# Optimization experiments

Hardware: AMD Instinct MI355X
Metric: run time of the kernel (lower is better)

Reference implementation:

```python
import jax, jax.numpy as jnp
import numpy as np

NUM_CLASSES = 80
ROI_SIZE = 7
SAMPLING = 2          # RoIAlign sampling_ratio
STRIDES = (4, 8, 16, 32)
FINEST_SCALE = 56.0
SCORE_THR = 0.05
IOU_THR = 0.5
MAX_PER_IMG = 100
MEANS = jnp.zeros((4,), jnp.float32)
STDS = jnp.array([0.1, 0.1, 0.2, 0.2], jnp.float32)
MAX_RATIO = abs(float(np.log(16.0 / 1000.0)))


def setup_inputs() -> dict:
    key = jax.random.key(0)
    ks = jax.random.split(key, 20)
    C, H0, W0 = 256, 200, 336
    inp = {}
    for i in range(4):
        inp[f"feat{i}"] = jax.random.normal(ks[i], (1, C, H0 >> i, W0 >> i), jnp.float32)
    N = 1000
    IMG_W, IMG_H = 1344.0, 800.0
    cx = jax.random.uniform(ks[4], (N,), minval=0.0, maxval=IMG_W)
    cy = jax.random.uniform(ks[5], (N,), minval=0.0, maxval=IMG_H)
    w = jax.random.uniform(ks[6], (N,), minval=16.0, maxval=512.0)
    h = jax.random.uniform(ks[7], (N,), minval=16.0, maxval=512.0)
    x1 = jnp.clip(cx - w / 2, 0.0, IMG_W - 1)
    y1 = jnp.clip(cy - h / 2, 0.0, IMG_H - 1)
    x2 = jnp.clip(cx + w / 2, x1 + 1.0, IMG_W)
    y2 = jnp.clip(cy + h / 2, y1 + 1.0, IMG_H)
    inp["proposals"] = jnp.stack([x1, y1, x2, y2], axis=-1)
    D = C * ROI_SIZE * ROI_SIZE  # 12544
    FC = 1024
    inp["fc1_w"] = 0.01 * jax.random.normal(ks[8], (FC, D), jnp.float32)
    inp["fc1_b"] = jnp.zeros((FC,), jnp.float32)
    inp["fc2_w"] = 0.01 * jax.random.normal(ks[9], (FC, FC), jnp.float32)
    inp["fc2_b"] = jnp.zeros((FC,), jnp.float32)
    inp["cls_w"] = 0.01 * jax.random.normal(ks[10], (NUM_CLASSES + 1, FC), jnp.float32)
    inp["cls_b"] = jnp.zeros((NUM_CLASSES + 1,), jnp.float32)
    inp["reg_w"] = 0.01 * jax.random.normal(ks[11], (NUM_CLASSES * 4, FC), jnp.float32)
    inp["reg_b"] = jnp.zeros((NUM_CLASSES * 4,), jnp.float32)
    return inp


def _roi_align(feat, rois, scale):
    # feat [C,H,W]; rois [N,4]; aligned RoIAlign, 7x7 out, sampling_ratio=2
    C, H, W = feat.shape
    P = ROI_SIZE * SAMPLING  # 14 uniform sample points per axis

    def one(roi):
        x1, y1, x2, y2 = roi[0], roi[1], roi[2], roi[3]
        sx = x1 * scale - 0.5
        sy = y1 * scale - 0.5
        rw = (x2 - x1) * scale
        rh = (y2 - y1) * scale
        pts = (jnp.arange(P, dtype=feat.dtype) + 0.5) / P
        xs = sx + pts * rw
        ys = sy + pts * rh
        y0 = jnp.floor(ys)
        x0 = jnp.floor(xs)
        ly = ys - y0
        lx = xs - x0
        y0i = jnp.clip(y0.astype(jnp.int32), 0, H - 1)
        y1i = jnp.clip(y0i + 1, 0, H - 1)
        x0i = jnp.clip(x0.astype(jnp.int32), 0, W - 1)
        x1i = jnp.clip(x0i + 1, 0, W - 1)
        g = lambda yi, xi: feat[:, yi[:, None], xi[None, :]]  # [C,P,P]
        ly_ = ly[None, :, None]
        lx_ = lx[None, None, :]
        val = (1 - ly_) * ((1 - lx_) * g(y0i, x0i) + lx_ * g(y0i, x1i)) \
            + ly_ * ((1 - lx_) * g(y1i, x0i) + lx_ * g(y1i, x1i))
        vy = ((ys >= -1.0) & (ys <= H))[None, :, None]
        vx = ((xs >= -1.0) & (xs <= W))[None, None, :]
        val = jnp.where(vy & vx, val, 0.0)
        # average-pool the 2x2 samples per bin -> [C,7,7]
        return val.reshape(C, ROI_SIZE, SAMPLING, ROI_SIZE, SAMPLING).mean(axis=(2, 4))

    return jax.vmap(one)(rois)  # [N,C,7,7]


def _delta2bbox(proposals, deltas):
    d = deltas.reshape(-1, NUM_CLASSES, 4) * STDS + MEANS
    dx, dy = d[..., 0], d[..., 1]
    dw = jnp.clip(d[..., 2], -MAX_RATIO, MAX_RATIO)
    dh = jnp.clip(d[..., 3], -MAX_RATIO, MAX_RATIO)
    px = ((proposals[:, 0] + proposals[:, 2]) * 0.5)[:, None]
    py = ((proposals[:, 1] + proposals[:, 3]) * 0.5)[:, None]
    pw = (proposals[:, 2] - proposals[:, 0])[:, None]
    ph = (proposals[:, 3] - proposals[:, 1])[:, None]
    gw = pw * jnp.exp(dw)
    gh = ph * jnp.exp(dh)
    gx = px + pw * dx
    gy = py + ph * dy
    return jnp.stack([gx - gw * 0.5, gy - gh * 0.5, gx + gw * 0.5, gy + gh * 0.5], axis=-1)


def _pairwise_iou(b):
    x1, y1, x2, y2 = b[:, 0], b[:, 1], b[:, 2], b[:, 3]
    area = jnp.maximum(x2 - x1, 0.0) * jnp.maximum(y2 - y1, 0.0)
    iw = jnp.maximum(jnp.minimum(x2[:, None], x2[None, :]) - jnp.maximum(x1[:, None], x1[None, :]), 0.0)
    ih = jnp.maximum(jnp.minimum(y2[:, None], y2[None, :]) - jnp.maximum(y1[:, None], y1[None, :]), 0.0)
    inter = iw * ih
    return inter / jnp.maximum(area[:, None] + area[None, :] - inter, 1e-8)


def _nms_one_class(boxes, scores):
    # greedy NMS, static shapes; returns score-sorted boxes/scores + keep mask
    N = scores.shape[0]
    order = jnp.argsort(-scores)
    b = boxes[order]
    s = scores[order]
    iou = _pairwise_iou(b)
    idx = jnp.arange(N)

    def body(i, keep):
        sup = (iou[i] > IOU_THR) & keep[i] & (idx > i)
        return keep & jnp.logical_not(sup)

    keep = jax.lax.fori_loop(0, N, body, s > SCORE_THR)
    return b, s, keep


def _batched_nms(bboxes, scores):
    # bboxes [N,81,4], scores [N,81]; class 80 is background (skipped)
    cls_boxes = jnp.transpose(bboxes[:, :NUM_CLASSES, :], (1, 0, 2))  # [80,N,4]
    cls_scores = scores[:, :NUM_CLASSES].T                            # [80,N]
    b, s, keep = jax.vmap(_nms_one_class)(cls_boxes, cls_scores)
    N = s.shape[1]
    s_flat = jnp.where(keep, s, -1.0).reshape(-1)
    topv, topi = jax.lax.top_k(s_flat, MAX_PER_IMG)
    det_boxes = b.reshape(-1, 4)[topi]
    det_classes = (topi // N).astype(jnp.int32)
    valid = topv > 0.0
    num_det = valid.sum().astype(jnp.int32)
    det_scores = jnp.where(valid, topv, 0.0)
    det_boxes = jnp.where(valid[:, None], det_boxes, 0.0)
    det_classes = jnp.where(valid, det_classes, -1)
    return num_det, det_boxes[None], det_scores[None], det_classes[None]


def _forward(feat0, feat1, feat2, feat3, proposals,
             fc1_w, fc1_b, fc2_w, fc2_b, cls_w, cls_b, reg_w, reg_b):
    feats = [feat0[0], feat1[0], feat2[0], feat3[0]]
    wp = proposals[:, 2] - proposals[:, 0]
    hp = proposals[:, 3] - proposals[:, 1]
    scale = jnp.sqrt(jnp.maximum(wp * hp, 1e-6))
    lvl = jnp.clip(jnp.floor(jnp.log2(scale / FINEST_SCALE + 1e-6)), 0, 3).astype(jnp.int32)
    N = proposals.shape[0]
    C = feats[0].shape[0]
    roi_feats = jnp.zeros((N, C, ROI_SIZE, ROI_SIZE), proposals.dtype)
    for l, stride in enumerate(STRIDES):
        f = _roi_align(feats[l], proposals, 1.0 / stride)
        roi_feats = jnp.where((lvl == l)[:, None, None, None], f, roi_feats)
    h = roi_feats.reshape(N, -1)
    h = jax.nn.relu(h @ fc1_w.T + fc1_b)
    h = jax.nn.relu(h @ fc2_w.T + fc2_b)
    cls_score = h @ cls_w.T + cls_b          # [N,81]
    bbox_pred = h @ reg_w.T + reg_b          # [N,320]
    scores = jax.nn.softmax(cls_score, axis=1)
    boxes = _delta2bbox(proposals, bbox_pred)                          # [N,80,4]
    boxes = jnp.concatenate([boxes, jnp.zeros((N, 1, 4), boxes.dtype)], axis=1)
    return _batched_nms(boxes, scores)


def reference(feat0, feat1, feat2, feat3, proposals,
              fc1_w, fc1_b, fc2_w, fc2_b, cls_w, cls_b, reg_w, reg_b):
    return _forward(feat0, feat1, feat2, feat3, proposals,
                    fc1_w, fc1_b, fc2_w, fc2_b, cls_w, cls_b, reg_w, reg_b)
```

## Files before the change

### kernel.cpp

```cpp
#include <hip/hip_runtime.h>
#include <math.h>

#define NCLS   80
#define NPROP  1000
#define FCDIM  1024
#define DFLAT  12544
#define MPAD   1024
#define MAXR   4.1351665567423560f
#define LDSP   40
#define NMSW   16
#define NCAT   404

#define CSPLIT 8
#define CG     (256 / CSPLIT)

typedef unsigned short ushort_t;
typedef unsigned long long ull_t;
using short8  = __attribute__((ext_vector_type(8))) short;
using float4v = __attribute__((ext_vector_type(4))) float;

__device__ inline ushort_t f2bf(float f) {
    unsigned int u = __float_as_uint(f);
    unsigned int r = (u + 0x7fffu + ((u >> 16) & 1u)) >> 16;
    return (ushort_t)r;
}

__device__ __forceinline__ unsigned cvtpk_bf16(float lo, float hi) {
    unsigned r;
    asm("v_cvt_pk_bf16_f32 %0, %1, %2" : "=v"(r) : "v"(lo), "v"(hi));
    return r;
}

__global__ __launch_bounds__(256) void roi_align_k(
    const float* __restrict__ f0, const float* __restrict__ f1,
    const float* __restrict__ f2, const float* __restrict__ f3,
    const float* __restrict__ props, ushort_t* __restrict__ Abf)
{
    int r  = blockIdx.x;
    int cz = blockIdx.y;
    int t  = threadIdx.x;

    if (r >= NPROP) {
        for (int i = t; i < CG * 49; i += 256)
            Abf[(size_t)r * DFLAT + cz * (CG * 49) + i] = 0;
        return;
    }

    const float4 p = *(const float4*)&props[(size_t)r * 4];
    float wp = p.z - p.x, hp = p.w - p.y;
    float scale = sqrtf(fmaxf(wp * hp, 1e-6f));
    int lvl = (int)floorf(log2f(scale / 56.0f + 1e-6f));
    lvl = min(max(lvl, 0), 3);

    const float* f; int H, W; float sc;
    switch (lvl) {
        case 0:  f = f0; H = 200; W = 336; sc = 0.25f;    break;
        case 1:  f = f1; H = 100; W = 168; sc = 0.125f;   break;
        case 2:  f = f2; H = 50;  W = 84;  sc = 0.0625f;  break;
        default: f = f3; H = 25;  W = 42;  sc = 0.03125f; break;
    }

    if (t >= 196) return;

    int b   = t >> 2;
    int sub = t & 3;
    int by = b / 7, bx = b - by * 7;
    int sy = by * 2 + (sub >> 1);
    int sx = bx * 2 + (sub & 1);

    float startx = p.x * sc - 0.5f, rangex = (p.z - p.x) * sc;
    float starty = p.y * sc - 0.5f, rangey = (p.w - p.y) * sc;
    float posx = startx + (((float)sx + 0.5f) / 14.0f) * rangex;
    float posy = starty + (((float)sy + 0.5f) / 14.0f) * rangey;

    float flx = floorf(posx), fly = floorf(posy);
    float lx = posx - flx, ly = posy - fly;
    int x0 = min(max((int)flx, 0), W - 1);
    int y0 = min(max((int)fly, 0), H - 1);
    int y1 = min(y0 + 1, H - 1);
    bool valid = (posx >= -1.0f) && (posx <= (float)W) &&
                 (posy >= -1.0f) && (posy <= (float)H);
    float vm = valid ? 0.25f : 0.0f;

    float w00 = (1.f - ly) * (1.f - lx) * vm;
    float w01 = (1.f - ly) * lx * vm;
    float w10 = ly * (1.f - lx) * vm;
    float w11 = ly * lx * vm;

    int  xb = min(x0, W - 2);
    bool xr = (x0 == W - 1);
    float wtA = xr ? 0.f : w00, wtB = xr ? (w00 + w01) : w01;
    float wbA = xr ? 0.f : w10, wbB = xr ? (w10 + w11) : w11;
    int ot = y0 * W + xb;
    int ob = y1 * W + xb;

    const int HW = H * W;
    ushort_t* orow = Abf + (size_t)r * DFLAT + cz * (CG * 49);
    const float* pl = f + (size_t)(cz * CG) * HW;

    #pragma unroll 8
    for (int c = 0; c < CG; c++) {
        float2 tv = *(const float2*)(pl + ot);
        float2 bv = *(const float2*)(pl + ob);
        float v = tv.x * wtA + tv.y * wtB + bv.x * wbA + bv.y * wbB;
        v += __shfl_xor(v, 1);
        v += __shfl_xor(v, 2);
        if (sub == 0)
            orow[c * 49 + b] = f2bf(v);
        pl += HW;
    }
}

__global__ __launch_bounds__(256) void gemm_sk_k(
    const ushort_t* __restrict__ A, const float* __restrict__ Wf,
    float* __restrict__ P, int N, int K, int KC)
{
    __shared__ ushort_t As[2][128 * LDSP];
    __shared__ ushort_t Bs[2][128 * LDSP];

    int tid = threadIdx.x;
    int w = tid >> 6, l = tid & 63;
    int wm = (w >> 1) * 64, wn = (w & 1) * 64;

    int bid = (int)blockIdx.x + (int)gridDim.x * ((int)blockIdx.y + (int)gridDim.y * (int)blockIdx.z);
    int bx = bid & 7;
    int slot = bid >> 3;
    int by = slot % (int)gridDim.y;
    int bz = slot / (int)gridDim.y;

    int m0 = by * 128, n0 = bx * 128;
    int kc0 = bz * KC;

    int lrow = tid >> 2;
    int lko  = (tid & 3) * 8;

    const ushort_t* Ag = A  + (size_t)(m0 + lrow) * K + kc0 + lko;
    const float*    Wg = Wf + (size_t)(n0 + lrow) * K + kc0 + lko;
    size_t rowK64 = (size_t)64 * K;

    float4v acc[4][4];
    #pragma unroll
    for (int i = 0; i < 4; i++)
        #pragma unroll
        for (int j = 0; j < 4; j++)
            acc[i][j] = (float4v){0.f, 0.f, 0.f, 0.f};

    int rl = l & 15, q = l >> 4;

    {
        uint4  a0  = *(const uint4*)(Ag);
        uint4  a1  = *(const uint4*)(Ag + rowK64);
        float4 w0a = *(const float4*)(Wg);
        float4 w0b = *(const float4*)(Wg + 4);
        float4 w1a = *(const float4*)(Wg + rowK64);
        float4 w1b = *(const float4*)(Wg + rowK64 + 4);
        uint4 wv0, wv1;
        wv0.x = cvtpk_bf16(w0a.x, w0a.y); wv0.y = cvtpk_bf16(w0a.z, w0a.w);
        wv0.z = cvtpk_bf16(w0b.x, w0b.y); wv0.w = cvtpk_bf16(w0b.z, w0b.w);
        wv1.x = cvtpk_bf16(w1a.x, w1a.y); wv1.y = cvtpk_bf16(w1a.z, w1a.w);
        wv1.z = cvtpk_bf16(w1b.x, w1b.y); wv1.w = cvtpk_bf16(w1b.z, w1b.w);
        *(uint4*)&As[0][lrow * LDSP + lko]        = a0;
        *(uint4*)&As[0][(lrow + 64) * LDSP + lko] = a1;
        *(uint4*)&Bs[0][lrow * LDSP + lko]        = wv0;
        *(uint4*)&Bs[0][(lrow + 64) * LDSP + lko] = wv1;
    }
    __syncthreads();

    int cur = 0;
    for (int k0 = 0; k0 < KC; k0 += 32) {
        bool more = (k0 + 32) < KC;

        uint4 na0, na1;
        float4 nw0a, nw0b, nw1a, nw1b;
        if (more) {
            na0  = *(const uint4*)(Ag + k0 + 32);
            na1  = *(const uint4*)(Ag + rowK64 + k0 + 32);
            nw0a = *(const float4*)(Wg + k0 + 32);
            nw0b = *(const float4*)(Wg + k0 + 36);
            nw1a = *(const float4*)(Wg + rowK64 + k0 + 32);
            nw1b = *(const float4*)(Wg + rowK64 + k0 + 36);
        }

        const ushort_t* Ac = As[cur];
        const ushort_t* Bc = Bs[cur];
        short8 af[4], bfr[4];
        #pragma unroll
        for (int i = 0; i < 4; i++)
            af[i] = *(const short8*)&Ac[(wm + i * 16 + rl) * LDSP + q * 8];
        #pragma unroll
        for (int j = 0; j < 4; j++)
            bfr[j] = *(const short8*)&Bc[(wn + j * 16 + rl) * LDSP + q * 8];

        #pragma unroll
        for (int i = 0; i < 4; i++)
            #pragma unroll
            for (int j = 0; j < 4; j++)
                acc[i][j] = __builtin_amdgcn_mfma_f32_16x16x32_bf16(
                    af[i], bfr[j], acc[i][j], 0, 0, 0);

        if (more) {
            uint4 wv0, wv1;
            wv0.x = cvtpk_bf16(nw0a.x, nw0a.y); wv0.y = cvtpk_bf16(nw0a.z, nw0a.w);
            wv0.z = cvtpk_bf16(nw0b.x, nw0b.y); wv0.w = cvtpk_bf16(nw0b.z, nw0b.w);
            wv1.x = cvtpk_bf16(nw1a.x, nw1a.y); wv1.y = cvtpk_bf16(nw1a.z, nw1a.w);
            wv1.z = cvtpk_bf16(nw1b.x, nw1b.y); wv1.w = cvtpk_bf16(nw1b.z, nw1b.w);
            ushort_t* An = As[cur ^ 1];
            ushort_t* Bn = Bs[cur ^ 1];
            *(uint4*)&An[lrow * LDSP + lko]        = na0;
            *(uint4*)&An[(lrow + 64) * LDSP + lko] = na1;
            *(uint4*)&Bn[lrow * LDSP + lko]        = wv0;
            *(uint4*)&Bn[(lrow + 64) * LDSP + lko] = wv1;
        }

        __syncthreads();
        cur ^= 1;
    }

    float* Pz = P + (size_t)bz * ((size_t)MPAD * N);
    #pragma unroll
    for (int i = 0; i < 4; i++) {
        #pragma unroll
        for (int j = 0; j < 4; j++) {
            int col = n0 + wn + j * 16 + rl;
            #pragma unroll
            for (int rr = 0; rr < 4; rr++) {
                int row = m0 + wm + i * 16 + q * 4 + rr;
                Pz[(size_t)row * N + col] = acc[i][j][rr];
            }
        }
    }
}

__global__ __launch_bounds__(256) void reduce_sk_k(
    const float* __restrict__ P, const float* __restrict__ bias,
    void* __restrict__ Cout, int N, int SK, int relu, int out_bf16)
{
    size_t idx = ((size_t)blockIdx.x * 256 + threadIdx.x) * 4;
    float4 s = *(const float4*)&P[idx];
    for (int z = 1; z < SK; z++) {
        float4 pv = *(const float4*)&P[(size_t)z * ((size_t)MPAD * N) + idx];
        s.x += pv.x; s.y += pv.y; s.z += pv.z; s.w += pv.w;
    }
    int n = (int)(idx % N);
    float4 b = *(const float4*)&bias[n];
    s.x += b.x; s.y += b.y; s.z += b.z; s.w += b.w;
    if (relu) {
        s.x = fmaxf(s.x, 0.f); s.y = fmaxf(s.y, 0.f);
        s.z = fmaxf(s.z, 0.f); s.w = fmaxf(s.w, 0.f);
    }
    if (out_bf16) {
        ushort4 o;
        o.x = f2bf(s.x); o.y = f2bf(s.y); o.z = f2bf(s.z); o.w = f2bf(s.w);
        *(ushort4*)&((ushort_t*)Cout)[idx] = o;
    } else {
        *(float4*)&((float*)Cout)[idx] = s;
    }
}

__global__ __launch_bounds__(256) void concat_w_k(
    const float* __restrict__ reg_w, const float* __restrict__ cls_w,
    const float* __restrict__ reg_b, const float* __restrict__ cls_b,
    float* __restrict__ Wcat, float* __restrict__ bcat)
{
    int row = blockIdx.x;
    int t = threadIdx.x;
    float4 v = make_float4(0.f, 0.f, 0.f, 0.f);
    float bv = 0.f;
    if (row < 320) {
        v = *(const float4*)&reg_w[(size_t)row * FCDIM + t * 4];
        bv = reg_b[row];
    } else if (row < NCAT - 3) {
        v = *(const float4*)&cls_w[(size_t)(row - 320) * FCDIM + t * 4];
        bv = cls_b[row - 320];
    }
    *(float4*)&Wcat[(size_t)row * FCDIM + t * 4] = v;
    if (t == 0) bcat[row] = bv;
}

__global__ __launch_bounds__(256) void gemm_tn_k(
    const float* __restrict__ A, const float* __restrict__ W,
    const float* __restrict__ bias, float* __restrict__ C,
    int M, int N, int K, int relu)
{
    __shared__ float As[16][64];
    __shared__ float Bs[16][64];

    int tid = threadIdx.x;
    int tx = tid & 15;
    int ty = tid >> 4;
    int m0 = blockIdx.y * 64, n0 = blockIdx.x * 64;

    int lr = tid >> 2;
    int lk = (tid & 3) << 2;

    const float* Arow = A + (size_t)(m0 + lr) * K + lk;
    const float* Wrow = W + (size_t)(n0 + lr) * K + lk;
    bool mOK = (m0 + lr) < M;
    bool nOK = (n0 + lr) < N;

    float acc[4][4] = {};

    for (int k0 = 0; k0 < K; k0 += 16) {
        float4 av = mOK ? *(const float4*)(Arow + k0) : make_float4(0.f, 0.f, 0.f, 0.f);
        float4 wv = nOK ? *(const float4*)(Wrow + k0) : make_float4(0.f, 0.f, 0.f, 0.f);
        As[lk + 0][lr] = av.x; As[lk + 1][lr] = av.y;
        As[lk + 2][lr] = av.z; As[lk + 3][lr] = av.w;
        Bs[lk + 0][lr] = wv.x; Bs[lk + 1][lr] = wv.y;
        Bs[lk + 2][lr] = wv.z; Bs[lk + 3][lr] = wv.w;
        __syncthreads();

        #pragma unroll
        for (int kk = 0; kk < 16; kk++) {
            float4 a = *(const float4*)&As[kk][ty << 2];
            float4 b = *(const float4*)&Bs[kk][tx << 2];
            acc[0][0] += a.x * b.x; acc[0][1] += a.x * b.y;
            acc[0][2] += a.x * b.z; acc[0][3] += a.x * b.w;
            acc[1][0] += a.y * b.x; acc[1][1] += a.y * b.y;
            acc[1][2] += a.y * b.z; acc[1][3] += a.y * b.w;
            acc[2][0] += a.z * b.x; acc[2][1] += a.z * b.y;
            acc[2][2] += a.z * b.z; acc[2][3] += a.z * b.w;
            acc[3][0] += a.w * b.x; acc[3][1] += a.w * b.y;
            acc[3][2] += a.w * b.z; acc[3][3] += a.w * b.w;
        }
        __syncthreads();
    }

    #pragma unroll
    for (int i = 0; i < 4; i++) {
        int m = m0 + (ty << 2) + i;
        if (m >= M) continue;
        #pragma unroll
        for (int j = 0; j < 4; j++) {
            int n = n0 + (tx << 2) + j;
            if (n < N) {
                float v = acc[i][j] + bias[n];
                if (relu) v = fmaxf(v, 0.f);
                C[(size_t)m * N + n] = v;
            }
        }
    }
}

__global__ __launch_bounds__(128) void head_post_k(
    const float* __restrict__ hr_s, const float* __restrict__ props,
    float* __restrict__ probsT, float* __restrict__ boxesT)
{
    int r = blockIdx.x, t = threadIdx.x;
    __shared__ float red[128];

    float x = (t < 81) ? hr_s[(size_t)r * NCAT + 320 + t] : -1e30f;
    red[t] = x; __syncthreads();
    for (int s = 64; s > 0; s >>= 1) {
        if (t < s) red[t] = fmaxf(red[t], red[t + s]);
        __syncthreads();
    }
    float mx = red[0];
    __syncthreads();

    float e = (t < 81) ? expf(x - mx) : 0.f;
    red[t] = e; __syncthreads();
    for (int s = 64; s > 0; s >>= 1) {
        if (t < s) red[t] += red[t + s];
        __syncthreads();
    }
    float inv = 1.f / red[0];

    if (t < NCLS) {
        probsT[(size_t)t * NPROP + r] = e * inv;

        const float4 p = *(const float4*)&props[(size_t)r * 4];
        float4 d = *(const float4*)&hr_s[(size_t)r * NCAT + t * 4];
        float dx = d.x * 0.1f, dy = d.y * 0.1f;
        float dw = fminf(fmaxf(d.z * 0.2f, -MAXR), MAXR);
        float dh = fminf(fmaxf(d.w * 0.2f, -MAXR), MAXR);
        float px = (p.x + p.z) * 0.5f, py = (p.y + p.w) * 0.5f;
        float pw = p.z - p.x, ph = p.w - p.y;
        float gw = pw * expf(dw), gh = ph * expf(dh);
        float gx = px + pw * dx, gy = py + ph * dy;
        float4 bo = make_float4(gx - gw * 0.5f, gy - gh * 0.5f,
                                gx + gw * 0.5f, gy + gh * 0.5f);
        *(float4*)&boxesT[(size_t)(t * NPROP + r) * 4] = bo;
    }
}

__global__ __launch_bounds__(512) void sort_k(
    const float* __restrict__ probsT, const float* __restrict__ boxesT,
    float* __restrict__ sortedS, float* __restrict__ sortedB)
{
    int c = blockIdx.x, t = threadIdx.x;
    __shared__ float sk[1024];
    __shared__ int   si[1024];

    for (int j = t; j < 1024; j += 512) {
        sk[j] = (j < NPROP) ? probsT[(size_t)c * NPROP + j] : -1e30f;
        si[j] = j;
    }
    __syncthreads();

    for (int size = 2; size <= 1024; size <<= 1) {
        for (int stride = size >> 1; stride > 0; stride >>= 1) {
            int i = (t << 1) - (t & (stride - 1));
            int j = i + stride;
            float ka = sk[i], kb = sk[j];
            int ia = si[i], ib = si[j];
            bool aFirst = (ka > kb) || (ka == kb && ia < ib);
            bool desc = ((i & size) == 0);
            if (desc ? !aFirst : aFirst) {
                sk[i] = kb; sk[j] = ka; si[i] = ib; si[j] = ia;
            }
            __syncthreads();
        }
    }

    for (int j = t; j < NPROP; j += 512) {
        sortedS[(size_t)c * NPROP + j] = sk[j];
        const float4 bb = *(const float4*)&boxesT[(size_t)(c * NPROP + si[j]) * 4];
        *(float4*)&sortedB[(size_t)(c * NPROP + j) * 4] = bb;
    }
}

__global__ __launch_bounds__(256) void nms_k(
    const float* __restrict__ sortedS, const float* __restrict__ sortedB,
    ull_t* __restrict__ masks, float* __restrict__ candS, int* __restrict__ candI)
{
    int c = blockIdx.x, t = threadIdx.x;
    __shared__ float x1s[NPROP], y1s[NPROP], x2s[NPROP], y2s[NPROP], ars[NPROP];
    __shared__ unsigned char kp[NPROP];
    __shared__ int segc[256];

    for (int j = t; j < NPROP; j += 256) {
        float4 b = *(const float4*)&sortedB[(size_t)(c * NPROP + j) * 4];
        x1s[j] = b.x; y1s[j] = b.y; x2s[j] = b.z; y2s[j] = b.w;
        ars[j] = fmaxf(b.z - b.x, 0.f) * fmaxf(b.w - b.y, 0.f);
        kp[j] = sortedS[(size_t)c * NPROP + j] > 0.05f ? 1 : 0;
    }
    __syncthreads();

    ull_t* M = masks + (size_t)c * NPROP * NMSW;
    for (int i = t; i < NPROP; i += 256) {
        if (!kp[i]) continue;
        float xi1 = x1s[i], yi1 = y1s[i], xi2 = x2s[i], yi2 = y2s[i], ai = ars[i];
        for (int w = 0; w < NMSW; w++) {
            ull_t m = 0ull;
            int j0 = w << 6;
            #pragma unroll 4
            for (int k = 0; k < 64; k++) {
                int j = j0 + k;
                if (j < NPROP) {
                    float iw = fmaxf(fminf(xi2, x2s[j]) - fmaxf(xi1, x1s[j]), 0.f);
                    float ih = fmaxf(fminf(yi2, y2s[j]) - fmaxf(yi1, y1s[j]), 0.f);
                    float inter = iw * ih;
                    float iou = inter / fmaxf(ai + ars[j] - inter, 1e-8f);
                    if (iou > 0.5f) m |= (1ull << k);
                }
            }
            M[(size_t)i * NMSW + w] = m;
        }
    }
    __syncthreads();

    if (t < 64) {
        ull_t rem = 0ull;
        for (int i = 0; i < NPROP; i++) {
            if (kp[i]) {
                ull_t w = __shfl(rem, i >> 6);
                if ((w >> (i & 63)) & 1ull) {
                    if (t == 0) kp[i] = 0;
                } else {
                    if (t < NMSW) rem |= M[(size_t)i * NMSW + t];
                }
            }
        }
    }
    __syncthreads();

    int j0 = t * 4;
    int cnt = 0;
    #pragma unroll
    for (int k = 0; k < 4; k++) {
        int j = j0 + k;
        if (j < NPROP && kp[j]) cnt++;
    }
    segc[t] = cnt;
    __syncthreads();
    for (int off = 1; off < 256; off <<= 1) {
        int add = (t >= off) ? segc[t - off] : 0;
        __syncthreads();
        segc[t] += add;
        __syncthreads();
    }
    int pos = segc[t] - cnt;
    #pragma unroll
    for (int k = 0; k < 4; k++) {
        int j = j0 + k;
        if (j < NPROP && kp[j]) {
            if (pos < 100) {
                candS[c * 100 + pos] = sortedS[(size_t)c * NPROP + j];
                candI[c * 100 + pos] = c * NPROP + j;
            }
            pos++;
        }
    }
    int total = segc[255];
    for (int p = total + t; p < 100; p += 256) {
        candS[c * 100 + p] = -2e30f;
        candI[c * 100 + p] = 0x7fffffff;
    }
}

__global__ __launch_bounds__(128) void merge_k(
    const float* __restrict__ candS, const int* __restrict__ candI,
    const float* __restrict__ sortedB, float* __restrict__ out)
{
    int t = threadIdx.x;
    __shared__ int   head[NCLS];
    __shared__ float topv[100];
    __shared__ int   topi[100];

    if (t < NCLS) head[t] = 0;
    __syncthreads();

    for (int r = 0; r < 100; r++) {
        if (t < 64) {
            float v = -2e30f; int fi = 0x7fffffff; int cls = 0;
            {
                int h = head[t];
                if (h < 100) { v = candS[t * 100 + h]; fi = candI[t * 100 + h]; cls = t; }
            }
            int c2 = t + 64;
            if (c2 < NCLS) {
                int h = head[c2];
                if (h < 100) {
                    float v2 = candS[c2 * 100 + h]; int fi2 = candI[c2 * 100 + h];
                    if (v2 > v || (v2 == v && fi2 < fi)) { v = v2; fi = fi2; cls = c2; }
                }
            }
            #pragma unroll
            for (int s = 1; s < 64; s <<= 1) {
                float ov = __shfl_xor(v, s);
                int ofi  = __shfl_xor(fi, s);
                int ocl  = __shfl_xor(cls, s);
                if (ov > v || (ov == v && ofi < fi)) { v = ov; fi = ofi; cls = ocl; }
            }
            if (t == 0) { topv[r] = v; topi[r] = fi; head[cls]++; }
        }
        __syncthreads();
    }

    if (t < 100) {
        float v = topv[t]; int fi = topi[t];
        bool valid = v > 0.0f;
        float4 bb = make_float4(0.f, 0.f, 0.f, 0.f);
        if (valid) bb = *(const float4*)&sortedB[(size_t)fi * 4];
        out[1 + t * 4 + 0] = bb.x;
        out[1 + t * 4 + 1] = bb.y;
        out[1 + t * 4 + 2] = bb.z;
        out[1 + t * 4 + 3] = bb.w;
        out[401 + t] = valid ? v : 0.0f;
        out[501 + t] = valid ? (float)(fi / NPROP) : -1.0f;
    }
    if (t == 0) {
        int n = 0;
        for (int r = 0; r < 100; r++) n += (topv[r] > 0.0f) ? 1 : 0;
        out[0] = (float)n;
    }
}

extern "C" void kernel_launch(void* const* d_in, const int* in_sizes, int n_in,
                              void* d_out, int out_size, void* d_ws, size_t ws_size,
                              hipStream_t stream)
{
    const float* f0    = (const float*)d_in[0];
    const float* f1    = (const float*)d_in[1];
    const float* f2    = (const float*)d_in[2];
    const float* f3    = (const float*)d_in[3];
    const float* props = (const float*)d_in[4];
    const float* fc1_w = (const float*)d_in[5];
    const float* fc1_b = (const float*)d_in[6];
    const float* fc2_w = (const float*)d_in[7];
    const float* fc2_b = (const float*)d_in[8];
    const float* cls_w = (const float*)d_in[9];
    const float* cls_b = (const float*)d_in[10];
    const float* reg_w = (const float*)d_in[11];
    const float* reg_b = (const float*)d_in[12];
    float* out = (float*)d_out;

    unsigned char* base = (unsigned char*)d_ws;
    ushort_t* Abf  = (ushort_t*)(base);
    ushort_t* h1   = (ushort_t*)(base + 25690112);
    float*    P1   = (float*)(base + 27787264);
    float*    P2   = (float*)(base + 27787264);
    float*    h2   = (float*)(base + 44564480);
    float*    hr_s    = (float*)(base + 48758784);
    float*    probsT  = (float*)(base + 50401280);
    float*    boxesT  = (float*)(base + 50721280);
    float*    sortedS = (float*)(base + 52001280);
    float*    sortedB = (float*)(base + 52321280);
    float*    candS   = (float*)(base + 53601280);
    int*      candI   = (int*)(base + 53633280);
    float*    Wcat    = (float*)(base + 53665280);
    float*    bcat    = (float*)(base + 55320064);
    ull_t*    masks   = (ull_t*)(base);

    roi_align_k<<<dim3(MPAD, CSPLIT), 256, 0, stream>>>(f0, f1, f2, f3, props, Abf);

    gemm_sk_k<<<dim3(FCDIM / 128, MPAD / 128, 8), 256, 0, stream>>>(
        Abf, fc1_w, P1, FCDIM, DFLAT, DFLAT / 8);
    reduce_sk_k<<<(MPAD * FCDIM / 4) / 256, 256, 0, stream>>>(
        P1, fc1_b, h1, FCDIM, 8, 1, 1);

    concat_w_k<<<NCAT, 256, 0, stream>>>(reg_w, cls_w, reg_b, cls_b, Wcat, bcat);

    gemm_sk_k<<<dim3(FCDIM / 128, MPAD / 128, 4), 256, 0, stream>>>(
        h1, fc2_w, P2, FCDIM, FCDIM, FCDIM / 4);
    reduce_sk_k<<<(MPAD * FCDIM / 4) / 256, 256, 0, stream>>>(
        P2, fc2_b, h2, FCDIM, 4, 1, 0);

    gemm_tn_k<<<dim3((NCAT + 63) / 64, (NPROP + 63) / 64), 256, 0, stream>>>(
        h2, Wcat, bcat, hr_s, NPROP, NCAT, FCDIM, 0);

    head_post_k<<<NPROP, 128, 0, stream>>>(hr_s, props, probsT, boxesT);
    sort_k<<<NCLS, 512, 0, stream>>>(probsT, boxesT, sortedS, sortedB);
    nms_k<<<NCLS, 256, 0, stream>>>(sortedS, sortedB, masks, candS, candI);
    merge_k<<<1, 128, 0, stream>>>(candS, candI, sortedB, out);
}
```

Before: 565.9 us.

## Transpose FPN features to bf16 NHWC before RoIAlign for coalesced channel gathers

Adds a transpose kernel that converts all four feature levels into a channel-last bf16 buffer, done in two 128-channel halves that reuse workspace space. A new RoIAlign kernel precomputes sample offsets and weights in LDS, then has threads read adjacent channels of each bilinear corner, so gathers become coalesced instead of strided across NCHW planes. In exchange, the whole feature pyramid (about 89k pixels by 256 channels) is read and rewritten on every call, and the launch count rises from one to four. Features are rounded to bf16 before interpolation, which adds some precision loss.

```diff
diff --git a/kernel.cpp b/kernel.cpp
--- a/kernel.cpp
+++ b/kernel.cpp
@@ -10,9 +10,8 @@
 #define LDSP   40
 #define NMSW   16
 #define NCAT   404
-
-#define CSPLIT 8
-#define CG     (256 / CSPLIT)
+#define NPIX   89250
+#define HCH    128
 
 typedef unsigned short ushort_t;
 typedef unsigned long long ull_t;
@@ -24,6 +23,9 @@
     unsigned int r = (u + 0x7fffu + ((u >> 16) & 1u)) >> 16;
     return (ushort_t)r;
 }
+__device__ inline float bf2f(ushort_t u) {
+    return __uint_as_float(((unsigned int)u) << 16);
+}
 
 __device__ __forceinline__ unsigned cvtpk_bf16(float lo, float hi) {
     unsigned r;
@@ -31,84 +33,119 @@
     return r;
 }
 
-__global__ __launch_bounds__(256) void roi_align_k(
+__global__ __launch_bounds__(256) void nhwc_k(
     const float* __restrict__ f0, const float* __restrict__ f1,
     const float* __restrict__ f2, const float* __restrict__ f3,
-    const float* __restrict__ props, ushort_t* __restrict__ Abf)
-{
-    int r  = blockIdx.x;
-    int cz = blockIdx.y;
-    int t  = threadIdx.x;
+    int half, ushort_t* __restrict__ Fh)
+{
+    int pt = blockIdx.x;
+    const float* src; int HW, loff, p0;
+    if (pt < 2100)      { src = f0; HW = 67200; loff = 0;     p0 = pt * 32; }
+    else if (pt < 2625) { src = f1; HW = 16800; loff = 67200; p0 = (pt - 2100) * 32; }
+    else if (pt < 2757) { src = f2; HW = 4200;  loff = 84000; p0 = (pt - 2625) * 32; }
+    else                { src = f3; HW = 1050;  loff = 88200; p0 = (pt - 2757) * 32; }
+
+    int tx = threadIdx.x, ty = threadIdx.y;
+    int cbase = half * HCH + blockIdx.y * 32;
+    __shared__ float tile[32][33];
+
+    #pragma unroll
+    for (int i = 0; i < 4; i++) {
+        int cy = ty + i * 8;
+        int p  = p0 + tx;
+        tile[cy][tx] = (p < HW) ? src[(size_t)(cbase + cy) * HW + p] : 0.f;
+    }
+    __syncthreads();
+    #pragma unroll
+    for (int i = 0; i < 4; i++) {
+        int py = ty + i * 8;
+        int p  = p0 + py;
+        if (p < HW)
+            Fh[(size_t)(loff + p) * HCH + blockIdx.y * 32 + tx] = f2bf(tile[tx][py]);
+    }
+}
+
+__global__ __launch_bounds__(256) void roi_nhwc_k(
+    const float* __restrict__ props, const ushort_t* __restrict__ Fh,
+    int half, ushort_t* __restrict__ Abf)
+{
+    int r = blockIdx.x;
+    int t = threadIdx.x;
+    ushort_t* orow = Abf + (size_t)r * DFLAT + half * (HCH * 49);
 
     if (r >= NPROP) {
-        for (int i = t; i < CG * 49; i += 256)
-            Abf[(size_t)r * DFLAT + cz * (CG * 49) + i] = 0;
+        for (int i = t; i < HCH * 49; i += 256) orow[i] = 0;
         return;
     }
 
-    const float4 p = *(const float4*)&props[(size_t)r * 4];
-    float wp = p.z - p.x, hp = p.w - p.y;
-    float scale = sqrtf(fmaxf(wp * hp, 1e-6f));
-    int lvl = (int)floorf(log2f(scale / 56.0f + 1e-6f));
-    lvl = min(max(lvl, 0), 3);
-
-    const float* f; int H, W; float sc;
-    switch (lvl) {
-        case 0:  f = f0; H = 200; W = 336; sc = 0.25f;    break;
-        case 1:  f = f1; H = 100; W = 168; sc = 0.125f;   break;
-        case 2:  f = f2; H = 50;  W = 84;  sc = 0.0625f;  break;
-        default: f = f3; H = 25;  W = 42;  sc = 0.03125f; break;
-    }
-
-    if (t >= 196) return;
-
-    int b   = t >> 2;
-    int sub = t & 3;
-    int by = b / 7, bx = b - by * 7;
-    int sy = by * 2 + (sub >> 1);
-    int sx = bx * 2 + (sub & 1);
-
-    float startx = p.x * sc - 0.5f, rangex = (p.z - p.x) * sc;
-    float starty = p.y * sc - 0.5f, rangey = (p.w - p.y) * sc;
-    float posx = startx + (((float)sx + 0.5f) / 14.0f) * rangex;
-    float posy = starty + (((float)sy + 0.5f) / 14.0f) * rangey;
-
-    float flx = floorf(posx), fly = floorf(posy);
-    float lx = posx - flx, ly = posy - fly;
-    int x0 = min(max((int)flx, 0), W - 1);
-    int y0 = min(max((int)fly, 0), H - 1);
-    int y1 = min(y0 + 1, H - 1);
-    bool valid = (posx >= -1.0f) && (posx <= (float)W) &&
-                 (posy >= -1.0f) && (posy <= (float)H);
-    float vm = valid ? 0.25f : 0.0f;
-
-    float w00 = (1.f - ly) * (1.f - lx) * vm;
-    float w01 = (1.f - ly) * lx * vm;
-    float w10 = ly * (1.f - lx) * vm;
-    float w11 = ly * lx * vm;
-
-    int  xb = min(x0, W - 2);
-    bool xr = (x0 == W - 1);
-    float wtA = xr ? 0.f : w00, wtB = xr ? (w00 + w01) : w01;
-    float wbA = xr ? 0.f : w10, wbB = xr ? (w10 + w11) : w11;
-    int ot = y0 * W + xb;
-    int ob = y1 * W + xb;
-
-    const int HW = H * W;
-    ushort_t* orow = Abf + (size_t)r * DFLAT + cz * (CG * 49);
-    const float* pl = f + (size_t)(cz * CG) * HW;
-
-    #pragma unroll 8
-    for (int c = 0; c < CG; c++) {
-        float2 tv = *(const float2*)(pl + ot);
-        float2 bv = *(const float2*)(pl + ob);
-        float v = tv.x * wtA + tv.y * wtB + bv.x * wbA + bv.y * wbB;
-        v += __shfl_xor(v, 1);
-        v += __shfl_xor(v, 2);
-        if (sub == 0)
-            orow[c * 49 + b] = f2bf(v);
-        pl += HW;
-    }
+    __shared__ int4   offs[196];
+    __shared__ float4 wgts[196];
+    __shared__ ushort_t obuf[HCH * 49];
+
+    if (t < 196) {
+        const float4 p = *(const float4*)&props[(size_t)r * 4];
+        float wp = p.z - p.x, hp = p.w - p.y;
+        float scale = sqrtf(fmaxf(wp * hp, 1e-6f));
+        int lvl = (int)floorf(log2f(scale / 56.0f + 1e-6f));
+        lvl = min(max(lvl, 0), 3);
+
+        int H, W, loff; float sc;
+        switch (lvl) {
+            case 0:  H = 200; W = 336; sc = 0.25f;    loff = 0;     break;
+            case 1:  H = 100; W = 168; sc = 0.125f;   loff = 67200; break;
+            case 2:  H = 50;  W = 84;  sc = 0.0625f;  loff = 84000; break;
+            default: H = 25;  W = 42;  sc = 0.03125f; loff = 88200; break;
+        }
+
+        int b   = t >> 2;
+        int sub = t & 3;
+        int by = b / 7, bx = b - by * 7;
+        int sy = by * 2 + (sub >> 1);
+        int sx = bx * 2 + (sub & 1);
+
+        float startx = p.x * sc - 0.5f, rangex = (p.z - p.x) * sc;
+        float starty = p.y * sc - 0.5f, rangey = (p.w - p.y) * sc;
+        float posx = startx + (((float)sx + 0.5f) / 14.0f) * rangex;
+        float posy = starty + (((float)sy + 0.5f) / 14.0f) * rangey;
+
+        float flx = floorf(posx), fly = floorf(posy);
+        float lx = posx - flx, ly = posy - fly;
+        int x0 = min(max((int)flx, 0), W - 1);
+        int x1 = min(x0 + 1, W - 1);
+        int y0 = min(max((int)fly, 0), H - 1);
+        int y1 = min(y0 + 1, H - 1);
+        bool valid = (posx >= -1.0f) && (posx <= (float)W) &&
+                     (posy >= -1.0f) && (posy <= (float)H);
+        float vm = valid ? 0.25f : 0.0f;
+
+        wgts[t] = make_float4((1.f - ly) * (1.f - lx) * vm,
+                              (1.f - ly) * lx * vm,
+                              ly * (1.f - lx) * vm,
+                              ly * lx * vm);
+        offs[t] = make_int4((loff + y0 * W + x0) * HCH,
+                            (loff + y0 * W + x1) * HCH,
+                            (loff + y1 * W + x0) * HCH,
+                            (loff + y1 * W + x1) * HCH);
+    }
+    __syncthreads();
+
+    int c  = t & (HCH - 1);
+    int bg = t >> 7;
+    for (int b = bg; b < 49; b += 2) {
+        float acc = 0.f;
+        #pragma unroll
+        for (int s = 0; s < 4; s++) {
+            int4   o  = offs[b * 4 + s];
+            float4 wv = wgts[b * 4 + s];
+            acc += wv.x * bf2f(Fh[o.x + c]) + wv.y * bf2f(Fh[o.y + c])
+                 + wv.z * bf2f(Fh[o.z + c]) + wv.w * bf2f(Fh[o.w + c]);
+        }
+        obuf[c * 49 + b] = f2bf(acc);
+    }
+    __syncthreads();
+
+    for (int i = t; i < HCH * 49; i += 256)
+        orow[i] = obuf[i];
 }
 
 __global__ __launch_bounds__(256) void gemm_sk_k(
@@ -588,6 +625,7 @@
     unsigned char* base = (unsigned char*)d_ws;
     ushort_t* Abf  = (ushort_t*)(base);
     ushort_t* h1   = (ushort_t*)(base + 25690112);
+    ushort_t* Fh   = (ushort_t*)(base + 27787264);
     float*    P1   = (float*)(base + 27787264);
     float*    P2   = (float*)(base + 27787264);
     float*    h2   = (float*)(base + 44564480);
@@ -602,7 +640,10 @@
     float*    bcat    = (float*)(base + 55320064);
     ull_t*    masks   = (ull_t*)(base);
 
-    roi_align_k<<<dim3(MPAD, CSPLIT), 256, 0, stream>>>(f0, f1, f2, f3, props, Abf);
+    nhwc_k<<<dim3(2790, 4), dim3(32, 8), 0, stream>>>(f0, f1, f2, f3, 0, Fh);
+    roi_nhwc_k<<<MPAD, 256, 0, stream>>>(props, Fh, 0, Abf);
+    nhwc_k<<<dim3(2790, 4), dim3(32, 8), 0, stream>>>(f0, f1, f2, f3, 1, Fh);
+    roi_nhwc_k<<<MPAD, 256, 0, stream>>>(props, Fh, 1, Abf);
 
     gemm_sk_k<<<dim3(FCDIM / 128, MPAD / 128, 8), 256, 0, stream>>>(
         Abf, fc1_w, P1, FCDIM, DFLAT, DFLAT / 8);
```

Measured after the change: 634.8 us. 1.12x slower.
